# Kernel optimization log

Measured on AMD Instinct MI355X. Metric: run time of the kernel, lower is better.

The kernel has to match this reference:

```python
import jax, jax.numpy as jnp
import numpy as np

IN_FEATURES = 4096
OUT_FEATURES = 11008
GROUP_SIZE = 128


def setup_inputs() -> dict:
    key = jax.random.key(0)
    k_x, k_w, k_s, k_z, k_b = jax.random.split(key, 5)
    x = jax.random.normal(k_x, (8, IN_FEATURES), dtype=jnp.float32)
    # packed INT4 weights: two 4-bit values per byte, stored in int32 (0..255)
    weight_q = jax.random.randint(k_w, (OUT_FEATURES, IN_FEATURES // 2), 0, 256, dtype=jnp.int32)
    num_groups = IN_FEATURES // GROUP_SIZE  # 32
    scales = jax.random.uniform(k_s, (OUT_FEATURES, num_groups), dtype=jnp.float32) * 0.01 + 1e-4
    zeros = jax.random.normal(k_z, (OUT_FEATURES, num_groups), dtype=jnp.float32) * 0.05
    bias = jax.random.normal(k_b, (OUT_FEATURES,), dtype=jnp.float32) * 0.02
    return {"x": x, "weight_q": weight_q, "scales": scales, "zeros": zeros, "bias": bias}


def _dequantize(weight_q, scales, zeros):
    # unpack INT4: low nibble first, then high nibble (matches torch stack order)
    low = weight_q & 15
    high = (weight_q >> 4) & 15
    q = jnp.stack([low, high], axis=-1).reshape(OUT_FEATURES, -1)  # [out, in]
    q = q.astype(scales.dtype)
    num_groups = scales.shape[1]
    q = q[:, : num_groups * GROUP_SIZE].reshape(OUT_FEATURES, num_groups, GROUP_SIZE)
    w = q * scales[:, :, None] + zeros[:, :, None]
    return w.reshape(OUT_FEATURES, -1)[:, :IN_FEATURES]


def reference(x, weight_q, scales, zeros, bias):
    w = _dequantize(weight_q, scales, zeros)            # [out, in]
    return x.astype(w.dtype) @ w.T + bias               # [B, out]
```

## Files before the change

kernel.cpp:

```cpp
#include <hip/hip_runtime.h>

typedef _Float16 f16;
typedef __attribute__((ext_vector_type(2))) _Float16 f16x2;
typedef __attribute__((ext_vector_type(8))) _Float16 f16x8;
typedef __attribute__((ext_vector_type(4))) float f32x4;
typedef __attribute__((ext_vector_type(4))) unsigned u32x4;

constexpr int IN_F  = 4096;
constexpr int OUT_F = 11008;
constexpr int NGRP  = 32;
constexpr int NTILE = OUT_F / 16;
constexpr int PLANE = OUT_F * 8;

__device__ __forceinline__ unsigned dq2(unsigned q, f16x2 sp, f16x2 zp) {
    unsigned t = (((q << 12) | q) & 0x000F000Fu) | 0x64006400u;
    f16x2 u = __builtin_bit_cast(f16x2, t);
    u = u - (f16x2){(_Float16)1024.0f, (_Float16)1024.0f};
    u = u * sp + zp;
    return __builtin_bit_cast(unsigned, u);
}

__device__ __forceinline__ f16x2 bcast(float v) {
    _Float16 h = (_Float16)v;
    return (f16x2){h, h};
}

__global__ __launch_bounds__(256, 4)
void qlin_partial(const int* __restrict__ wq,
                  const float* __restrict__ scales,
                  const float* __restrict__ zeros,
                  const float* __restrict__ xf,
                  float* __restrict__ wsf)
{
    __shared__ unsigned char wlds[4][8192];
    __shared__ f32x4 red[4][64];

    const int tid  = threadIdx.x;
    const int wv   = tid >> 6;
    const int lane = tid & 63;
    const int col  = lane & 15;
    const int kg   = lane >> 4;
    const int bid  = blockIdx.x;
    const int kq   = bid & 3;
    const int ot   = bid >> 2;
    const int o0   = ot * 16;
    const int orow = o0 + col;
    const bool mvalid = (col < 8);

    const int k0 = kq * 1024 + wv * 256;
    const int g0 = k0 >> 7;

    const f16x2 sp0 = bcast(scales[(size_t)orow * NGRP + g0]);
    const f16x2 sp1 = bcast(scales[(size_t)orow * NGRP + g0 + 1]);
    const f16x2 zp0 = bcast(zeros [(size_t)orow * NGRP + g0]);
    const f16x2 zp1 = bcast(zeros [(size_t)orow * NGRP + g0 + 1]);

    const char* wb = (const char*)wq;
    #pragma unroll
    for (int c = 0; c < 8; ++c) {
        const int r    = 2 * c + (lane >> 5);
        const size_t grow = (size_t)(o0 + r);
        const char* src = wb + grow * 8192 + (size_t)k0 * 2
                          + (((lane & 31) * 16) ^ ((r & 7) << 4));
        __builtin_amdgcn_global_load_lds(
            (const __attribute__((address_space(1))) void*)src,
            (__attribute__((address_space(3))) void*)&wlds[wv][c * 1024],
            16, 0, 0);
    }

    float4 xr[16];
    if (mvalid) {
        const float* xp = xf + (size_t)col * IN_F + k0 + kg * 8;
        #pragma unroll
        for (int t = 0; t < 8; ++t) {
            xr[2 * t]     = *(const float4*)(xp + t * 32);
            xr[2 * t + 1] = *(const float4*)(xp + t * 32 + 4);
        }
    } else {
        #pragma unroll
        for (int i = 0; i < 16; ++i) xr[i] = (float4){0.f, 0.f, 0.f, 0.f};
    }

    asm volatile("s_waitcnt vmcnt(0)" ::: "memory");
    __builtin_amdgcn_sched_barrier(0);

    const unsigned swz = (unsigned)((col & 7) << 4);
    const unsigned base = (unsigned)(wv * 8192 + col * 512);
    const unsigned char* lf = &wlds[0][0];

    f32x4 acc = {0.f, 0.f, 0.f, 0.f};
    #pragma unroll
    for (int t = 0; t < 8; ++t) {
        f16x8 af = (f16x8){(f16)xr[2*t].x,   (f16)xr[2*t].y,   (f16)xr[2*t].z,   (f16)xr[2*t].w,
                           (f16)xr[2*t+1].x, (f16)xr[2*t+1].y, (f16)xr[2*t+1].z, (f16)xr[2*t+1].w};
        const unsigned off = base + (((unsigned)(t * 64 + kg * 16)) ^ swz);
        const int4 q = *(const int4*)(lf + off);
        const f16x2 s2 = (t < 4) ? sp0 : sp1;
        const f16x2 z2 = (t < 4) ? zp0 : zp1;
        u32x4 bw = {dq2((unsigned)q.x, s2, z2),
                    dq2((unsigned)q.y, s2, z2),
                    dq2((unsigned)q.z, s2, z2),
                    dq2((unsigned)q.w, s2, z2)};
        f16x8 bfr = __builtin_bit_cast(f16x8, bw);
        acc = __builtin_amdgcn_mfma_f32_16x16x32_f16(af, bfr, acc, 0, 0, 0);
    }

    red[wv][lane] = acc;
    __syncthreads();

    if (tid < 64) {
        f32x4 ssum = red[0][tid];
        #pragma unroll
        for (int w = 1; w < 4; ++w) ssum += red[w][tid];
        const int n = tid & 15;
        const int mbase = (tid >> 4) * 4;
        if (mbase < 8) {
            float* plane = wsf + (size_t)kq * PLANE;
            #pragma unroll
            for (int i = 0; i < 4; ++i)
                plane[(size_t)(mbase + i) * OUT_F + o0 + n] = ssum[i];
        }
    }
}

__global__ __launch_bounds__(256)
void reduce_kernel(const float* __restrict__ wsf,
                   const float* __restrict__ bias,
                   float* __restrict__ out)
{
    const int idx = blockIdx.x * 256 + threadIdx.x;
    const int o = idx % OUT_F;
    out[idx] = bias[o] + wsf[idx] + wsf[PLANE + idx]
             + wsf[2 * PLANE + idx] + wsf[3 * PLANE + idx];
}

__global__ __launch_bounds__(256, 4)
void qlin_kernel(const int* __restrict__ wq,
                 const float* __restrict__ scales,
                 const float* __restrict__ zeros,
                 const float* __restrict__ bias,
                 const float* __restrict__ xf,
                 float* __restrict__ out)
{
    __shared__ unsigned char wlds[2][16][1024];
    __shared__ f32x4 red[4][64];

    const int tid  = threadIdx.x;
    const int wv   = tid >> 6;
    const int lane = tid & 63;
    const int col  = lane & 15;
    const int kg   = lane >> 4;
    const int o0   = blockIdx.x * 16;
    const int orow = o0 + col;
    const bool mvalid = (col < 8);

    f16x2 sp[8], zp[8];
    #pragma unroll
    for (int s = 0; s < 8; ++s) {
        sp[s] = bcast(scales[(size_t)orow * NGRP + s * 4 + wv]);
        zp[s] = bcast(zeros [(size_t)orow * NGRP + s * 4 + wv]);
    }

    const char* wtile = (const char*)wq + (size_t)o0 * 8192;
    auto stage = [&](int sl, int bufi) {
        #pragma unroll
        for (int c = 0; c < 4; ++c) {
            const int r = 4 * wv + c;
            const char* src = wtile + (size_t)r * 8192 + sl * 1024
                              + ((lane * 16) ^ ((r & 7) << 4));
            __builtin_amdgcn_global_load_lds(
                (const __attribute__((address_space(1))) void*)src,
                (__attribute__((address_space(3))) void*)&wlds[bufi][r][0],
                16, 0, 0);
        }
    };

    stage(0, 0);
    stage(1, 1);

    const float* xfcol = xf + (size_t)col * IN_F;
    const unsigned swz = (unsigned)((col & 7) << 4);
    f32x4 acc = {0.f, 0.f, 0.f, 0.f};

    #pragma unroll
    for (int s = 0; s < 8; ++s) {
        asm volatile("s_waitcnt vmcnt(0)" ::: "memory");
        __builtin_amdgcn_s_barrier();
        asm volatile("" ::: "memory");

        const f16x2 s2 = sp[s], z2 = zp[s];
        #pragma unroll
        for (int t = 0; t < 4; ++t) {
            const int k = s * 512 + wv * 128 + t * 32 + kg * 8;
            f16x8 af = (f16x8){0,0,0,0,0,0,0,0};
            if (mvalid) {
                float4 a0 = *(const float4*)(xfcol + k);
                float4 a1 = *(const float4*)(xfcol + k + 4);
                af = (f16x8){(f16)a0.x,(f16)a0.y,(f16)a0.z,(f16)a0.w,
                             (f16)a1.x,(f16)a1.y,(f16)a1.z,(f16)a1.w};
            }
            const unsigned off = ((unsigned)(wv * 256 + t * 64 + kg * 16)) ^ swz;
            const int4 q = *(const int4*)&wlds[s & 1][col][off];
            u32x4 bw = {dq2((unsigned)q.x, s2, z2),
                        dq2((unsigned)q.y, s2, z2),
                        dq2((unsigned)q.z, s2, z2),
                        dq2((unsigned)q.w, s2, z2)};
            f16x8 bfr = __builtin_bit_cast(f16x8, bw);
            acc = __builtin_amdgcn_mfma_f32_16x16x32_f16(af, bfr, acc, 0, 0, 0);
        }

        asm volatile("" ::: "memory");
        __builtin_amdgcn_s_barrier();
        if (s < 6) stage(s + 2, s & 1);
    }

    red[wv][lane] = acc;
    __syncthreads();

    if (tid < 64) {
        f32x4 ssum = red[0][tid];
        #pragma unroll
        for (int w = 1; w < 4; ++w) ssum += red[w][tid];
        const int n = tid & 15;
        const float bb = bias[o0 + n];
        const int mbase = (tid >> 4) * 4;
        if (mbase < 8) {
            #pragma unroll
            for (int i = 0; i < 4; ++i)
                out[(size_t)(mbase + i) * OUT_F + o0 + n] = ssum[i] + bb;
        }
    }
}

extern "C" void kernel_launch(void* const* d_in, const int* in_sizes, int n_in,
                              void* d_out, int out_size, void* d_ws, size_t ws_size,
                              hipStream_t stream) {
    const float* x  = (const float*)d_in[0];
    const int*   wq = (const int*)d_in[1];
    const float* sc = (const float*)d_in[2];
    const float* zr = (const float*)d_in[3];
    const float* bs = (const float*)d_in[4];
    float* out = (float*)d_out;
    (void)in_sizes; (void)n_in;

    if (ws_size >= (size_t)4 * PLANE * sizeof(float)) {
        float* wsf = (float*)d_ws;
        qlin_partial<<<NTILE * 4, 256, 0, stream>>>(wq, sc, zr, x, wsf);
        reduce_kernel<<<PLANE / 256, 256, 0, stream>>>(wsf, bs, out);
    } else {
        qlin_kernel<<<NTILE, 256, 0, stream>>>(wq, sc, zr, bs, x, out);
    }
}
```

Baseline: 27.67 us.

## Pipeline weight staging with double-buffered LDS and pre-convert activations to fp16

Splits each wave's weight tile into four stages that are double-buffered in LDS, issuing later global-to-LDS loads while earlier stages are dequantized and fed to MFMA. A separate prep kernel converts x to fp16 once, so the main kernel loads f16x8 fragments instead of converting from float registers. Scales and zeros are fetched as float2, and the reduction reuses the LDS buffer. The cost is an extra kernel launch and extra workspace, and the pipeline is shallow, so the overlap it can achieve may be limited.

```diff
diff --git a/kernel.cpp b/kernel.cpp
--- a/kernel.cpp
+++ b/kernel.cpp
@@ -2,6 +2,7 @@
 
 typedef _Float16 f16;
 typedef __attribute__((ext_vector_type(2))) _Float16 f16x2;
+typedef __attribute__((ext_vector_type(4))) _Float16 f16x4;
 typedef __attribute__((ext_vector_type(8))) _Float16 f16x8;
 typedef __attribute__((ext_vector_type(4))) float f32x4;
 typedef __attribute__((ext_vector_type(4))) unsigned u32x4;
@@ -25,15 +26,21 @@
     return (f16x2){h, h};
 }
 
+__global__ void xprep_kernel(const float* __restrict__ x, f16* __restrict__ xh) {
+    int i = (blockIdx.x * blockDim.x + threadIdx.x) * 4;
+    float4 v = *(const float4*)(x + i);
+    f16x4 r = {(f16)v.x, (f16)v.y, (f16)v.z, (f16)v.w};
+    *(f16x4*)(xh + i) = r;
+}
+
 __global__ __launch_bounds__(256, 4)
-void qlin_partial(const int* __restrict__ wq,
-                  const float* __restrict__ scales,
-                  const float* __restrict__ zeros,
-                  const float* __restrict__ xf,
-                  float* __restrict__ wsf)
+void qlin_pipe(const int* __restrict__ wq,
+               const float* __restrict__ scales,
+               const float* __restrict__ zeros,
+               const f16* __restrict__ xh,
+               float* __restrict__ wsf)
 {
-    __shared__ unsigned char wlds[4][8192];
-    __shared__ f32x4 red[4][64];
+    __shared__ unsigned char wlds[4][2][2048];
 
     const int tid  = threadIdx.x;
     const int wv   = tid >> 6;
@@ -45,81 +52,90 @@
     const int ot   = bid >> 2;
     const int o0   = ot * 16;
     const int orow = o0 + col;
+    const int k0   = kq * 1024 + wv * 256;
+    const int g0   = k0 >> 7;
     const bool mvalid = (col < 8);
 
-    const int k0 = kq * 1024 + wv * 256;
-    const int g0 = k0 >> 7;
-
-    const f16x2 sp0 = bcast(scales[(size_t)orow * NGRP + g0]);
-    const f16x2 sp1 = bcast(scales[(size_t)orow * NGRP + g0 + 1]);
-    const f16x2 zp0 = bcast(zeros [(size_t)orow * NGRP + g0]);
-    const f16x2 zp1 = bcast(zeros [(size_t)orow * NGRP + g0 + 1]);
-
-    const char* wb = (const char*)wq;
-    #pragma unroll
-    for (int c = 0; c < 8; ++c) {
-        const int r    = 2 * c + (lane >> 5);
-        const size_t grow = (size_t)(o0 + r);
-        const char* src = wb + grow * 8192 + (size_t)k0 * 2
-                          + (((lane & 31) * 16) ^ ((r & 7) << 4));
-        __builtin_amdgcn_global_load_lds(
-            (const __attribute__((address_space(1))) void*)src,
-            (__attribute__((address_space(3))) void*)&wlds[wv][c * 1024],
-            16, 0, 0);
-    }
-
-    float4 xr[16];
-    if (mvalid) {
-        const float* xp = xf + (size_t)col * IN_F + k0 + kg * 8;
-        #pragma unroll
-        for (int t = 0; t < 8; ++t) {
-            xr[2 * t]     = *(const float4*)(xp + t * 32);
-            xr[2 * t + 1] = *(const float4*)(xp + t * 32 + 4);
-        }
-    } else {
-        #pragma unroll
-        for (int i = 0; i < 16; ++i) xr[i] = (float4){0.f, 0.f, 0.f, 0.f};
-    }
-
-    asm volatile("s_waitcnt vmcnt(0)" ::: "memory");
-    __builtin_amdgcn_sched_barrier(0);
-
-    const unsigned swz = (unsigned)((col & 7) << 4);
-    const unsigned base = (unsigned)(wv * 8192 + col * 512);
-    const unsigned char* lf = &wlds[0][0];
-
+    float2 sg = *(const float2*)(scales + (size_t)orow * NGRP + g0);
+    float2 zg = *(const float2*)(zeros  + (size_t)orow * NGRP + g0);
+
+    f16x8 af[4][2];
+    const f16* xcol = xh + (size_t)col * IN_F + k0 + kg * 8;
+    #pragma unroll
+    for (int ss = 0; ss < 4; ++ss) {
+        if (mvalid) {
+            af[ss][0] = *(const f16x8*)(xcol + ss * 64);
+            af[ss][1] = *(const f16x8*)(xcol + ss * 64 + 32);
+        } else {
+            af[ss][0] = (f16x8){0,0,0,0,0,0,0,0};
+            af[ss][1] = (f16x8){0,0,0,0,0,0,0,0};
+        }
+    }
+
+    const char* wb   = (const char*)wq;
+    const int   coff = (lane & 7) * 16;
+
+    auto stageW = [&](int ss) {
+        const int b = ss & 1;
+        #pragma unroll
+        for (int j = 0; j < 2; ++j) {
+            const int r = j * 8 + (lane >> 3);
+            const char* src = wb + (size_t)(o0 + r) * 8192
+                              + (size_t)(k0 + ss * 64) * 2
+                              + (coff ^ ((r & 7) << 4));
+            __builtin_amdgcn_global_load_lds(
+                (const __attribute__((address_space(1))) void*)src,
+                (__attribute__((address_space(3))) void*)&wlds[wv][b][j * 1024],
+                16, 0, 0);
+        }
+    };
+
+    stageW(0); __builtin_amdgcn_sched_barrier(0);
+    stageW(1); __builtin_amdgcn_sched_barrier(0);
+
+    const unsigned rswz = (unsigned)((col & 7) << 4);
     f32x4 acc = {0.f, 0.f, 0.f, 0.f};
-    #pragma unroll
-    for (int t = 0; t < 8; ++t) {
-        f16x8 af = (f16x8){(f16)xr[2*t].x,   (f16)xr[2*t].y,   (f16)xr[2*t].z,   (f16)xr[2*t].w,
-                           (f16)xr[2*t+1].x, (f16)xr[2*t+1].y, (f16)xr[2*t+1].z, (f16)xr[2*t+1].w};
-        const unsigned off = base + (((unsigned)(t * 64 + kg * 16)) ^ swz);
-        const int4 q = *(const int4*)(lf + off);
-        const f16x2 s2 = (t < 4) ? sp0 : sp1;
-        const f16x2 z2 = (t < 4) ? zp0 : zp1;
-        u32x4 bw = {dq2((unsigned)q.x, s2, z2),
-                    dq2((unsigned)q.y, s2, z2),
-                    dq2((unsigned)q.z, s2, z2),
-                    dq2((unsigned)q.w, s2, z2)};
-        f16x8 bfr = __builtin_bit_cast(f16x8, bw);
-        acc = __builtin_amdgcn_mfma_f32_16x16x32_f16(af, bfr, acc, 0, 0, 0);
-    }
-
-    red[wv][lane] = acc;
+
+    #pragma unroll
+    for (int ss = 0; ss < 4; ++ss) {
+        if (ss < 3) asm volatile("s_waitcnt vmcnt(2)" ::: "memory");
+        else        asm volatile("s_waitcnt vmcnt(0)" ::: "memory");
+        __builtin_amdgcn_sched_barrier(0);
+
+        const unsigned char* buf = &wlds[wv][ss & 1][0];
+        const int4 qa = *(const int4*)(buf + (col * 128 + ((     kg * 16) ^ rswz)));
+        const int4 qb = *(const int4*)(buf + (col * 128 + ((64 + kg * 16) ^ rswz)));
+
+        asm volatile("s_waitcnt lgkmcnt(0)" ::: "memory");
+        __builtin_amdgcn_sched_barrier(0);
+        if (ss < 2) { stageW(ss + 2); __builtin_amdgcn_sched_barrier(0); }
+
+        const f16x2 s2 = bcast((ss < 2) ? sg.x : sg.y);
+        const f16x2 z2 = bcast((ss < 2) ? zg.x : zg.y);
+        u32x4 ba = {dq2((unsigned)qa.x, s2, z2), dq2((unsigned)qa.y, s2, z2),
+                    dq2((unsigned)qa.z, s2, z2), dq2((unsigned)qa.w, s2, z2)};
+        u32x4 bb = {dq2((unsigned)qb.x, s2, z2), dq2((unsigned)qb.y, s2, z2),
+                    dq2((unsigned)qb.z, s2, z2), dq2((unsigned)qb.w, s2, z2)};
+        acc = __builtin_amdgcn_mfma_f32_16x16x32_f16(af[ss][0],
+                __builtin_bit_cast(f16x8, ba), acc, 0, 0, 0);
+        acc = __builtin_amdgcn_mfma_f32_16x16x32_f16(af[ss][1],
+                __builtin_bit_cast(f16x8, bb), acc, 0, 0, 0);
+    }
+
+    *(f32x4*)&wlds[wv][0][lane * 16] = acc;
     __syncthreads();
 
-    if (tid < 64) {
-        f32x4 ssum = red[0][tid];
-        #pragma unroll
-        for (int w = 1; w < 4; ++w) ssum += red[w][tid];
+    if (tid < 32) {
+        f32x4 ssum = *(const f32x4*)&wlds[0][0][tid * 16];
+        #pragma unroll
+        for (int w = 1; w < 4; ++w)
+            ssum += *(const f32x4*)&wlds[w][0][tid * 16];
         const int n = tid & 15;
         const int mbase = (tid >> 4) * 4;
-        if (mbase < 8) {
-            float* plane = wsf + (size_t)kq * PLANE;
-            #pragma unroll
-            for (int i = 0; i < 4; ++i)
-                plane[(size_t)(mbase + i) * OUT_F + o0 + n] = ssum[i];
-        }
+        float* plane = wsf + (size_t)kq * PLANE;
+        #pragma unroll
+        for (int i = 0; i < 4; ++i)
+            plane[(size_t)(mbase + i) * OUT_F + o0 + n] = ssum[i];
     }
 }
 
@@ -243,9 +259,14 @@
     float* out = (float*)d_out;
     (void)in_sizes; (void)n_in;
 
-    if (ws_size >= (size_t)4 * PLANE * sizeof(float)) {
+    const size_t planes_b = (size_t)4 * PLANE * sizeof(float);
+    const size_t xh_b     = (size_t)8 * IN_F * sizeof(f16);
+
+    if (ws_size >= planes_b + xh_b) {
         float* wsf = (float*)d_ws;
-        qlin_partial<<<NTILE * 4, 256, 0, stream>>>(wq, sc, zr, x, wsf);
+        f16*   xh  = (f16*)((char*)d_ws + planes_b);
+        xprep_kernel<<<(8 * IN_F) / (256 * 4), 256, 0, stream>>>(x, xh);
+        qlin_pipe<<<NTILE * 4, 256, 0, stream>>>(wq, sc, zr, xh, wsf);
         reduce_kernel<<<PLANE / 256, 256, 0, stream>>>(wsf, bs, out);
     } else {
         qlin_kernel<<<NTILE, 256, 0, stream>>>(wq, sc, zr, bs, x, out);
```

Result: slower. 28.80 us (+4.1%).

## Add 8-way K-split GEMV path with fp16 x pre-conversion kernel

Applied to the files above, without the earlier changes.

Adds a new path with three kernels: one converts x to fp16 (padded to 16 rows) in workspace, one splits K eight ways so each wave handles a single quantization group with contiguous 1KB row bursts into LDS, and one reduces eight partial planes plus bias. Each block does less work and there are twice as many blocks, and x loads become half-width f16 vectors with no in-kernel conversion. In exchange it adds an extra kernel launch and doubles the partial-sum workspace traffic through the reduce.

```diff
diff --git a/kernel.cpp b/kernel.cpp
--- a/kernel.cpp
+++ b/kernel.cpp
@@ -2,6 +2,7 @@
 
 typedef _Float16 f16;
 typedef __attribute__((ext_vector_type(2))) _Float16 f16x2;
+typedef __attribute__((ext_vector_type(4))) _Float16 f16x4;
 typedef __attribute__((ext_vector_type(8))) _Float16 f16x8;
 typedef __attribute__((ext_vector_type(4))) float f32x4;
 typedef __attribute__((ext_vector_type(4))) unsigned u32x4;
@@ -23,6 +24,114 @@
 __device__ __forceinline__ f16x2 bcast(float v) {
     _Float16 h = (_Float16)v;
     return (f16x2){h, h};
+}
+
+__global__ void xprep16_kernel(const float* __restrict__ x, f16* __restrict__ xh) {
+    const int i4  = blockIdx.x * blockDim.x + threadIdx.x;
+    const int k4  = i4 * 4;
+    const int row = k4 >> 12;
+    const int kk  = k4 & 4095;
+    f16x4 r;
+    if (row < 8) {
+        float4 v = *(const float4*)(x + (size_t)row * IN_F + kk);
+        r = (f16x4){(f16)v.x, (f16)v.y, (f16)v.z, (f16)v.w};
+    } else {
+        r = (f16x4){0, 0, 0, 0};
+    }
+    *(f16x4*)(xh + (size_t)row * IN_F + kk) = r;
+}
+
+__global__ __launch_bounds__(256, 6)
+void qlin_rowburst(const int* __restrict__ wq,
+                   const float* __restrict__ scales,
+                   const float* __restrict__ zeros,
+                   const f16* __restrict__ xh,
+                   float* __restrict__ wsf)
+{
+    __shared__ unsigned char wlds[16][1024];
+
+    const int tid  = threadIdx.x;
+    const int wv   = tid >> 6;
+    const int lane = tid & 63;
+    const int col  = lane & 15;
+    const int kg   = lane >> 4;
+    const int bid  = blockIdx.x;
+    const int ot   = bid >> 3;
+    const int ks   = bid & 7;
+    const int o0   = ot * 16;
+    const int orow = o0 + col;
+    const int g    = ks * 4 + wv;
+
+    const float sgf = scales[(size_t)orow * NGRP + g];
+    const float zgf = zeros [(size_t)orow * NGRP + g];
+
+    const char* wb = (const char*)wq;
+    #pragma unroll
+    for (int j = 0; j < 4; ++j) {
+        const int r = 4 * wv + j;
+        const char* src = wb + (size_t)(o0 + r) * 8192 + (size_t)ks * 1024
+                          + (size_t)((lane ^ (r & 15)) & 63) * 16;
+        __builtin_amdgcn_global_load_lds(
+            (const __attribute__((address_space(1))) void*)src,
+            (__attribute__((address_space(3))) void*)&wlds[r][0],
+            16, 0, 0);
+    }
+
+    f16x8 af0, af1, af2, af3;
+    {
+        const f16* xp = xh + (size_t)col * IN_F + ks * 512 + wv * 128 + kg * 8;
+        af0 = *(const f16x8*)(xp);
+        af1 = *(const f16x8*)(xp + 32);
+        af2 = *(const f16x8*)(xp + 64);
+        af3 = *(const f16x8*)(xp + 96);
+    }
+
+    const f16x2 s2 = bcast(sgf);
+    const f16x2 z2 = bcast(zgf);
+
+    __syncthreads();
+
+    f32x4 acc = {0.f, 0.f, 0.f, 0.f};
+    #pragma unroll
+    for (int t = 0; t < 4; ++t) {
+        const int c = wv * 16 + t * 4 + kg;
+        const int4 q = *(const int4*)&wlds[col][((c ^ (col & 15)) & 63) * 16];
+        u32x4 bw = {dq2((unsigned)q.x, s2, z2), dq2((unsigned)q.y, s2, z2),
+                    dq2((unsigned)q.z, s2, z2), dq2((unsigned)q.w, s2, z2)};
+        const f16x8 bfr = __builtin_bit_cast(f16x8, bw);
+        const f16x8 afr = (t == 0) ? af0 : (t == 1) ? af1 : (t == 2) ? af2 : af3;
+        acc = __builtin_amdgcn_mfma_f32_16x16x32_f16(afr, bfr, acc, 0, 0, 0);
+    }
+
+    __syncthreads();
+    *(f32x4*)&wlds[0][0 + (size_t)(wv * 1024 + lane * 16)] = acc;
+    __syncthreads();
+
+    if (tid < 32) {
+        f32x4 ssum = *(const f32x4*)&wlds[0][tid * 16];
+        #pragma unroll
+        for (int w = 1; w < 4; ++w)
+            ssum += *(const f32x4*)&wlds[0][w * 1024 + tid * 16];
+        const int n = tid & 15;
+        const int mbase = (tid >> 4) * 4;
+        float* plane = wsf + (size_t)ks * PLANE;
+        #pragma unroll
+        for (int i = 0; i < 4; ++i)
+            plane[(size_t)(mbase + i) * OUT_F + o0 + n] = ssum[i];
+    }
+}
+
+__global__ __launch_bounds__(256)
+void reduce8_kernel(const float* __restrict__ wsf,
+                    const float* __restrict__ bias,
+                    float* __restrict__ out)
+{
+    const int idx = blockIdx.x * 256 + threadIdx.x;
+    const int o = idx % OUT_F;
+    float s = bias[o];
+    #pragma unroll
+    for (int p = 0; p < 8; ++p) s += wsf[(size_t)p * PLANE + idx];
+    out[idx] = s;
 }
 
 __global__ __launch_bounds__(256, 4)
@@ -58,9 +167,8 @@
     const char* wb = (const char*)wq;
     #pragma unroll
     for (int c = 0; c < 8; ++c) {
-        const int r    = 2 * c + (lane >> 5);
-        const size_t grow = (size_t)(o0 + r);
-        const char* src = wb + grow * 8192 + (size_t)k0 * 2
+        const int r = 2 * c + (lane >> 5);
+        const char* src = wb + (size_t)(o0 + r) * 8192 + (size_t)k0 * 2
                           + (((lane & 31) * 16) ^ ((r & 7) << 4));
         __builtin_amdgcn_global_load_lds(
             (const __attribute__((address_space(1))) void*)src,
@@ -84,7 +192,7 @@
     asm volatile("s_waitcnt vmcnt(0)" ::: "memory");
     __builtin_amdgcn_sched_barrier(0);
 
-    const unsigned swz = (unsigned)((col & 7) << 4);
+    const unsigned swz  = (unsigned)((col & 7) << 4);
     const unsigned base = (unsigned)(wv * 8192 + col * 512);
     const unsigned char* lf = &wlds[0][0];
 
@@ -97,10 +205,8 @@
         const int4 q = *(const int4*)(lf + off);
         const f16x2 s2 = (t < 4) ? sp0 : sp1;
         const f16x2 z2 = (t < 4) ? zp0 : zp1;
-        u32x4 bw = {dq2((unsigned)q.x, s2, z2),
-                    dq2((unsigned)q.y, s2, z2),
-                    dq2((unsigned)q.z, s2, z2),
-                    dq2((unsigned)q.w, s2, z2)};
+        u32x4 bw = {dq2((unsigned)q.x, s2, z2), dq2((unsigned)q.y, s2, z2),
+                    dq2((unsigned)q.z, s2, z2), dq2((unsigned)q.w, s2, z2)};
         f16x8 bfr = __builtin_bit_cast(f16x8, bw);
         acc = __builtin_amdgcn_mfma_f32_16x16x32_f16(af, bfr, acc, 0, 0, 0);
     }
@@ -124,9 +230,9 @@
 }
 
 __global__ __launch_bounds__(256)
-void reduce_kernel(const float* __restrict__ wsf,
-                   const float* __restrict__ bias,
-                   float* __restrict__ out)
+void reduce4_kernel(const float* __restrict__ wsf,
+                    const float* __restrict__ bias,
+                    float* __restrict__ out)
 {
     const int idx = blockIdx.x * 256 + threadIdx.x;
     const int o = idx % OUT_F;
@@ -243,10 +349,20 @@
     float* out = (float*)d_out;
     (void)in_sizes; (void)n_in;
 
-    if (ws_size >= (size_t)4 * PLANE * sizeof(float)) {
+    const size_t planes8_b = (size_t)8 * PLANE * sizeof(float);
+    const size_t planes4_b = (size_t)4 * PLANE * sizeof(float);
+    const size_t xh_b      = (size_t)16 * IN_F * sizeof(f16);
+
+    if (ws_size >= planes8_b + xh_b) {
+        float* wsf = (float*)d_ws;
+        f16*   xh  = (f16*)((char*)d_ws + planes8_b);
+        xprep16_kernel<<<(16 * IN_F) / (256 * 4), 256, 0, stream>>>(x, xh);
+        qlin_rowburst<<<NTILE * 8, 256, 0, stream>>>(wq, sc, zr, xh, wsf);
+        reduce8_kernel<<<PLANE / 256, 256, 0, stream>>>(wsf, bs, out);
+    } else if (ws_size >= planes4_b) {
         float* wsf = (float*)d_ws;
         qlin_partial<<<NTILE * 4, 256, 0, stream>>>(wq, sc, zr, x, wsf);
-        reduce_kernel<<<PLANE / 256, 256, 0, stream>>>(wsf, bs, out);
+        reduce4_kernel<<<PLANE / 256, 256, 0, stream>>>(wsf, bs, out);
     } else {
         qlin_kernel<<<NTILE, 256, 0, stream>>>(wq, sc, zr, bs, x, out);
     }
```

Measured after the change: 31.24 us. 1.13x slower.
